# Performance work log

Hardware: AMD Instinct MI355X
Metric: run time of the kernel (lower is better)

Reference implementation:

```python
import jax, jax.numpy as jnp
import numpy as np

N_NODES = 50000
N_EDGES = 1000000
NODE_DIM = 128
EDGE_DIM = 64


def setup_inputs() -> dict:
    key = jax.random.key(0)
    ks = jax.random.split(key, 12)
    s = 1.0 / np.sqrt(EDGE_DIM)
    sn = 1.0 / np.sqrt(NODE_DIM)
    return {
        "x": jax.random.normal(ks[0], (N_NODES, NODE_DIM), jnp.float32),
        "edge_index": jax.random.randint(ks[1], (2, N_EDGES), 0, N_NODES, jnp.int64),
        "edge_attr": jax.random.normal(ks[2], (N_EDGES, EDGE_DIM), jnp.float32),
        # lin_e: edge_dim -> edge_dim
        "We": jax.random.uniform(ks[3], (EDGE_DIM, EDGE_DIM), jnp.float32, -s, s),
        "be": jax.random.uniform(ks[4], (EDGE_DIM,), jnp.float32, -s, s),
        # lin_s: node_dim -> edge_dim
        "Ws": jax.random.uniform(ks[5], (EDGE_DIM, NODE_DIM), jnp.float32, -sn, sn),
        "bs": jax.random.uniform(ks[6], (EDGE_DIM,), jnp.float32, -sn, sn),
        # lin_t: node_dim -> edge_dim
        "Wt": jax.random.uniform(ks[7], (EDGE_DIM, NODE_DIM), jnp.float32, -sn, sn),
        "bt": jax.random.uniform(ks[8], (EDGE_DIM,), jnp.float32, -sn, sn),
        # lin1: edge_dim -> edge_dim
        "W1": jax.random.uniform(ks[9], (EDGE_DIM, EDGE_DIM), jnp.float32, -s, s),
        "b1": jax.random.uniform(ks[10], (EDGE_DIM,), jnp.float32, -s, s),
    }


def reference(x, edge_index, edge_attr, We, be, Ws, bs, Wt, bt, W1, b1):
    # node projections: [N, edge_dim]
    x_s = x @ Ws.T + bs
    x_t = x @ Wt.T + bt
    # fused edge update: lin_e(edge_attr) + gather(x_s, src) + gather(x_t, tgt)
    e = edge_attr @ We.T + be + x_s[edge_index[0]] + x_t[edge_index[1]]  # [E, edge_dim]
    e = jax.nn.gelu(e)
    return e @ W1.T + b1
```

## Files before the change

### kernel.cpp

```cpp
#include <hip/hip_runtime.h>
#include <stdint.h>

#define N_NODES_C 50000
#define N_EDGES_C 1000000
#define NODE_DIM_C 128
#define EDGE_DIM_C 64

typedef __attribute__((ext_vector_type(8))) short short8;
typedef __attribute__((ext_vector_type(4))) float floatx4;

__device__ __forceinline__ short f2bf(float f) {
    union { float f; uint32_t u; } v; v.f = f;
    uint32_t u = v.u;
    uint32_t r = (u + 0x7FFFu + ((u >> 16) & 1u)) >> 16;
    return (short)r;
}

__device__ __forceinline__ float gelu_tanh(float x) {
    float u = x * x;
    float inner = x * (1.0f + 0.044715f * u);
    float z = 1.5957691216057308f * inner;
    float ez = __expf(-z);
    return x / (1.0f + ez);
}

__global__ __launch_bounds__(256) void node_proj_kernel(
    const float* __restrict__ x,
    const float* __restrict__ Ws, const float* __restrict__ bs,
    const float* __restrict__ Wt, const float* __restrict__ bt,
    float* __restrict__ xs, float* __restrict__ xt)
{
    __shared__ __align__(16) short ws_frag[4][4][64][8];
    __shared__ __align__(16) short wt_frag[4][4][64][8];

    const int tid = threadIdx.x;
    for (int eidx = tid; eidx < 1024; eidx += 256) {
        int t = eidx >> 8;
        int s = (eidx >> 6) & 3;
        int l = eidx & 63;
        int n = t * 16 + (l & 15);
        int kb = s * 32 + ((l >> 4) << 3);
        const float* wsr = Ws + n * NODE_DIM_C + kb;
        const float* wtr = Wt + n * NODE_DIM_C + kb;
#pragma unroll
        for (int i = 0; i < 8; ++i) {
            ws_frag[t][s][l][i] = f2bf(wsr[i]);
            wt_frag[t][s][l][i] = f2bf(wtr[i]);
        }
    }
    __syncthreads();

    const int wave = tid >> 6, lane = tid & 63;
    const int m = lane & 15, q = lane >> 4;
    const int base = blockIdx.x * 64 + wave * 16;
    const int arow = base + m;

    floatx4 accS[4], accT[4];
    const floatx4 zero = {0.f, 0.f, 0.f, 0.f};
#pragma unroll
    for (int t = 0; t < 4; ++t) { accS[t] = zero; accT[t] = zero; }

#pragma unroll
    for (int s = 0; s < 4; ++s) {
        short8 a;
        if (arow < N_NODES_C) {
            const float4* ap = (const float4*)(x + arow * NODE_DIM_C + s * 32 + q * 8);
            float4 a0 = ap[0], a1 = ap[1];
            a[0] = f2bf(a0.x); a[1] = f2bf(a0.y); a[2] = f2bf(a0.z); a[3] = f2bf(a0.w);
            a[4] = f2bf(a1.x); a[5] = f2bf(a1.y); a[6] = f2bf(a1.z); a[7] = f2bf(a1.w);
        } else {
#pragma unroll
            for (int i = 0; i < 8; ++i) a[i] = 0;
        }
#pragma unroll
        for (int t = 0; t < 4; ++t) {
            short8 bS = *(const short8*)ws_frag[t][s][lane];
            short8 bT = *(const short8*)wt_frag[t][s][lane];
            accS[t] = __builtin_amdgcn_mfma_f32_16x16x32_bf16(a, bS, accS[t], 0, 0, 0);
            accT[t] = __builtin_amdgcn_mfma_f32_16x16x32_bf16(a, bT, accT[t], 0, 0, 0);
        }
    }

#pragma unroll
    for (int t = 0; t < 4; ++t) {
        int col = t * 16 + m;
        float bsv = bs[col], btv = bt[col];
#pragma unroll
        for (int r = 0; r < 4; ++r) {
            int n = base + q * 4 + r;
            if (n < N_NODES_C) {
                xs[n * EDGE_DIM_C + col] = accS[t][r] + bsv;
                xt[n * EDGE_DIM_C + col] = accT[t][r] + btv;
            }
        }
    }
}

__global__ __launch_bounds__(256) void edge_mlp_kernel(
    const float* __restrict__ ea, const int* __restrict__ ei,
    const float* __restrict__ We, const float* __restrict__ be,
    const float* __restrict__ W1, const float* __restrict__ b1,
    const float* __restrict__ xs, const float* __restrict__ xt,
    float* __restrict__ out)
{
    __shared__ __align__(16) short we_frag[4][2][64][8];
    __shared__ __align__(16) short w1_frag[4][2][64][8];
    __shared__ __align__(16) short pbuf[4][16][72];

    const int tid = threadIdx.x;
    for (int eidx = tid; eidx < 512; eidx += 256) {
        int t = eidx >> 7;
        int s = (eidx >> 6) & 1;
        int l = eidx & 63;
        int n = t * 16 + (l & 15);
        int kb = s * 32 + ((l >> 4) << 3);
        const float* wer = We + n * EDGE_DIM_C + kb;
        const float* w1r = W1 + n * EDGE_DIM_C + kb;
#pragma unroll
        for (int i = 0; i < 8; ++i) {
            we_frag[t][s][l][i] = f2bf(wer[i]);
            w1_frag[t][s][l][i] = f2bf(w1r[i]);
        }
    }
    __syncthreads();

    const int wave = tid >> 6, lane = tid & 63;
    const int m = lane & 15, q = lane >> 4;
    const int* __restrict__ src = ei;
    const int* __restrict__ tgt = ei + N_EDGES_C;

    float bev[4], b1v[4];
#pragma unroll
    for (int t = 0; t < 4; ++t) { bev[t] = be[t * 16 + m]; b1v[t] = b1[t * 16 + m]; }

    const floatx4 zero = {0.f, 0.f, 0.f, 0.f};
    const int nchunks = N_EDGES_C / 64;

    for (int chunk = blockIdx.x; chunk < nchunks; chunk += gridDim.x) {
        const int base = chunk * 64 + wave * 16;

        floatx4 acc[4];
#pragma unroll
        for (int t = 0; t < 4; ++t) acc[t] = zero;
#pragma unroll
        for (int s = 0; s < 2; ++s) {
            const float4* ap = (const float4*)(ea + (base + m) * EDGE_DIM_C + s * 32 + q * 8);
            float4 a0 = ap[0], a1 = ap[1];
            short8 a;
            a[0] = f2bf(a0.x); a[1] = f2bf(a0.y); a[2] = f2bf(a0.z); a[3] = f2bf(a0.w);
            a[4] = f2bf(a1.x); a[5] = f2bf(a1.y); a[6] = f2bf(a1.z); a[7] = f2bf(a1.w);
#pragma unroll
            for (int t = 0; t < 4; ++t) {
                short8 b = *(const short8*)we_frag[t][s][lane];
                acc[t] = __builtin_amdgcn_mfma_f32_16x16x32_bf16(a, b, acc[t], 0, 0, 0);
            }
        }

        int sidx[4], tidx[4];
#pragma unroll
        for (int r = 0; r < 4; ++r) {
            int e = base + q * 4 + r;
            int si = src[e], ti = tgt[e];
            sidx[r] = min(max(si, 0), N_NODES_C - 1);
            tidx[r] = min(max(ti, 0), N_NODES_C - 1);
        }
#pragma unroll
        for (int t = 0; t < 4; ++t) {
            int col = t * 16 + m;
#pragma unroll
            for (int r = 0; r < 4; ++r) {
                float c = acc[t][r] + bev[t]
                        + xs[sidx[r] * EDGE_DIM_C + col]
                        + xt[tidx[r] * EDGE_DIM_C + col];
                pbuf[wave][q * 4 + r][col] = f2bf(gelu_tanh(c));
            }
        }

        floatx4 acc2[4];
#pragma unroll
        for (int t = 0; t < 4; ++t) acc2[t] = zero;
#pragma unroll
        for (int s = 0; s < 2; ++s) {
            short8 a2 = *(const short8*)&pbuf[wave][m][s * 32 + q * 8];
#pragma unroll
            for (int t = 0; t < 4; ++t) {
                short8 b = *(const short8*)w1_frag[t][s][lane];
                acc2[t] = __builtin_amdgcn_mfma_f32_16x16x32_bf16(a2, b, acc2[t], 0, 0, 0);
            }
        }

#pragma unroll
        for (int t = 0; t < 4; ++t) {
            int col = t * 16 + m;
#pragma unroll
            for (int r = 0; r < 4; ++r) {
                int e = base + q * 4 + r;
                out[e * EDGE_DIM_C + col] = acc2[t][r] + b1v[t];
            }
        }
    }
}

extern "C" void kernel_launch(void* const* d_in, const int* in_sizes, int n_in,
                              void* d_out, int out_size, void* d_ws, size_t ws_size,
                              hipStream_t stream) {
    const float* x   = (const float*)d_in[0];
    const int*   ei  = (const int*)d_in[1];
    const float* ea  = (const float*)d_in[2];
    const float* We  = (const float*)d_in[3];
    const float* be  = (const float*)d_in[4];
    const float* Ws  = (const float*)d_in[5];
    const float* bs  = (const float*)d_in[6];
    const float* Wt  = (const float*)d_in[7];
    const float* bt  = (const float*)d_in[8];
    const float* W1  = (const float*)d_in[9];
    const float* b1  = (const float*)d_in[10];
    float* out = (float*)d_out;

    float* xs = (float*)d_ws;
    float* xt = xs + (size_t)N_NODES_C * EDGE_DIM_C;

    dim3 blk(256);
    dim3 grid_nodes((N_NODES_C + 63) / 64);
    node_proj_kernel<<<grid_nodes, blk, 0, stream>>>(x, Ws, bs, Wt, bt, xs, xt);

    dim3 grid_edges(3125);
    edge_mlp_kernel<<<grid_edges, blk, 0, stream>>>(ea, ei, We, be, W1, b1, xs, xt, out);
}
```

Before: 515.0 us.

## Store node projections in bf16, vectorize gathers and output via LDS staging

Node projections xs/xt are now stored as bf16, which halves the gather traffic. Each lane gathers full 16-element row segments with 16-byte loads instead of scalar strided loads. Edge indices for the next chunk are prefetched, the gathered sums are staged through shared memory, and the output tile is transposed through LDS so it can be written with float4 stores. It also adds an occupancy hint in the launch bounds, at the cost of extra LDS use and bf16 rounding of the projections.

```diff
diff --git a/kernel.cpp b/kernel.cpp
--- a/kernel.cpp
+++ b/kernel.cpp
@@ -14,6 +14,12 @@
     uint32_t u = v.u;
     uint32_t r = (u + 0x7FFFu + ((u >> 16) & 1u)) >> 16;
     return (short)r;
+}
+
+__device__ __forceinline__ float bf2f(short s) {
+    union { uint32_t u; float f; } v;
+    v.u = ((uint32_t)(uint16_t)s) << 16;
+    return v.f;
 }
 
 __device__ __forceinline__ float gelu_tanh(float x) {
@@ -28,7 +34,7 @@
     const float* __restrict__ x,
     const float* __restrict__ Ws, const float* __restrict__ bs,
     const float* __restrict__ Wt, const float* __restrict__ bt,
-    float* __restrict__ xs, float* __restrict__ xt)
+    ushort* __restrict__ xs, ushort* __restrict__ xt)
 {
     __shared__ __align__(16) short ws_frag[4][4][64][8];
     __shared__ __align__(16) short wt_frag[4][4][64][8];
@@ -64,7 +70,7 @@
     for (int s = 0; s < 4; ++s) {
         short8 a;
         if (arow < N_NODES_C) {
-            const float4* ap = (const float4*)(x + arow * NODE_DIM_C + s * 32 + q * 8);
+            const float4* ap = (const float4*)(x + (size_t)arow * NODE_DIM_C + s * 32 + q * 8);
             float4 a0 = ap[0], a1 = ap[1];
             a[0] = f2bf(a0.x); a[1] = f2bf(a0.y); a[2] = f2bf(a0.z); a[3] = f2bf(a0.w);
             a[4] = f2bf(a1.x); a[5] = f2bf(a1.y); a[6] = f2bf(a1.z); a[7] = f2bf(a1.w);
@@ -89,23 +95,24 @@
         for (int r = 0; r < 4; ++r) {
             int n = base + q * 4 + r;
             if (n < N_NODES_C) {
-                xs[n * EDGE_DIM_C + col] = accS[t][r] + bsv;
-                xt[n * EDGE_DIM_C + col] = accT[t][r] + btv;
-            }
-        }
-    }
-}
-
-__global__ __launch_bounds__(256) void edge_mlp_kernel(
+                xs[(size_t)n * EDGE_DIM_C + col] = (ushort)f2bf(accS[t][r] + bsv);
+                xt[(size_t)n * EDGE_DIM_C + col] = (ushort)f2bf(accT[t][r] + btv);
+            }
+        }
+    }
+}
+
+__global__ __launch_bounds__(256, 3) void edge_mlp_kernel(
     const float* __restrict__ ea, const int* __restrict__ ei,
     const float* __restrict__ We, const float* __restrict__ be,
     const float* __restrict__ W1, const float* __restrict__ b1,
-    const float* __restrict__ xs, const float* __restrict__ xt,
+    const ushort* __restrict__ xs, const ushort* __restrict__ xt,
     float* __restrict__ out)
 {
     __shared__ __align__(16) short we_frag[4][2][64][8];
     __shared__ __align__(16) short w1_frag[4][2][64][8];
     __shared__ __align__(16) short pbuf[4][16][72];
+    __shared__ __align__(16) float gsum[4][16][68];
 
     const int tid = threadIdx.x;
     for (int eidx = tid; eidx < 512; eidx += 256) {
@@ -126,6 +133,7 @@
 
     const int wave = tid >> 6, lane = tid & 63;
     const int m = lane & 15, q = lane >> 4;
+    const int g_r = lane >> 2, g_c = lane & 3;
     const int* __restrict__ src = ei;
     const int* __restrict__ tgt = ei + N_EDGES_C;
 
@@ -136,15 +144,32 @@
     const floatx4 zero = {0.f, 0.f, 0.f, 0.f};
     const int nchunks = N_EDGES_C / 64;
 
-    for (int chunk = blockIdx.x; chunk < nchunks; chunk += gridDim.x) {
+    int chunk = blockIdx.x;
+    int si = src[chunk * 64 + wave * 16 + g_r];
+    int ti = tgt[chunk * 64 + wave * 16 + g_r];
+
+    for (; chunk < nchunks; chunk += gridDim.x) {
         const int base = chunk * 64 + wave * 16;
 
+        int sic = min(max(si, 0), N_NODES_C - 1);
+        int tic = min(max(ti, 0), N_NODES_C - 1);
+        const short8* xsp = (const short8*)(xs + (size_t)sic * EDGE_DIM_C + g_c * 16);
+        const short8* xtp = (const short8*)(xt + (size_t)tic * EDGE_DIM_C + g_c * 16);
+        short8 gs0 = xsp[0], gs1 = xsp[1];
+        short8 gt0 = xtp[0], gt1 = xtp[1];
+
+        {
+            int en = min((chunk + (int)gridDim.x) * 64 + wave * 16 + g_r, N_EDGES_C - 1);
+            si = src[en];
+            ti = tgt[en];
+        }
+
         floatx4 acc[4];
 #pragma unroll
         for (int t = 0; t < 4; ++t) acc[t] = zero;
 #pragma unroll
         for (int s = 0; s < 2; ++s) {
-            const float4* ap = (const float4*)(ea + (base + m) * EDGE_DIM_C + s * 32 + q * 8);
+            const float4* ap = (const float4*)(ea + (size_t)(base + m) * EDGE_DIM_C + s * 32 + q * 8);
             float4 a0 = ap[0], a1 = ap[1];
             short8 a;
             a[0] = f2bf(a0.x); a[1] = f2bf(a0.y); a[2] = f2bf(a0.z); a[3] = f2bf(a0.w);
@@ -156,23 +181,29 @@
             }
         }
 
-        int sidx[4], tidx[4];
-#pragma unroll
-        for (int r = 0; r < 4; ++r) {
-            int e = base + q * 4 + r;
-            int si = src[e], ti = tgt[e];
-            sidx[r] = min(max(si, 0), N_NODES_C - 1);
-            tidx[r] = min(max(ti, 0), N_NODES_C - 1);
-        }
+        {
+            float* grow = &gsum[wave][g_r][g_c * 16];
+            float4 s0, s1, s2, s3;
+            s0.x = bf2f(gs0[0]) + bf2f(gt0[0]); s0.y = bf2f(gs0[1]) + bf2f(gt0[1]);
+            s0.z = bf2f(gs0[2]) + bf2f(gt0[2]); s0.w = bf2f(gs0[3]) + bf2f(gt0[3]);
+            s1.x = bf2f(gs0[4]) + bf2f(gt0[4]); s1.y = bf2f(gs0[5]) + bf2f(gt0[5]);
+            s1.z = bf2f(gs0[6]) + bf2f(gt0[6]); s1.w = bf2f(gs0[7]) + bf2f(gt0[7]);
+            s2.x = bf2f(gs1[0]) + bf2f(gt1[0]); s2.y = bf2f(gs1[1]) + bf2f(gt1[1]);
+            s2.z = bf2f(gs1[2]) + bf2f(gt1[2]); s2.w = bf2f(gs1[3]) + bf2f(gt1[3]);
+            s3.x = bf2f(gs1[4]) + bf2f(gt1[4]); s3.y = bf2f(gs1[5]) + bf2f(gt1[5]);
+            s3.z = bf2f(gs1[6]) + bf2f(gt1[6]); s3.w = bf2f(gs1[7]) + bf2f(gt1[7]);
+            ((float4*)grow)[0] = s0; ((float4*)grow)[1] = s1;
+            ((float4*)grow)[2] = s2; ((float4*)grow)[3] = s3;
+        }
+
 #pragma unroll
         for (int t = 0; t < 4; ++t) {
             int col = t * 16 + m;
 #pragma unroll
             for (int r = 0; r < 4; ++r) {
-                float c = acc[t][r] + bev[t]
-                        + xs[sidx[r] * EDGE_DIM_C + col]
-                        + xt[tidx[r] * EDGE_DIM_C + col];
-                pbuf[wave][q * 4 + r][col] = f2bf(gelu_tanh(c));
+                int row = q * 4 + r;
+                float c = acc[t][r] + bev[t] + gsum[wave][row][col];
+                pbuf[wave][row][col] = f2bf(gelu_tanh(c));
             }
         }
 
@@ -191,12 +222,16 @@
 
 #pragma unroll
         for (int t = 0; t < 4; ++t) {
-            int col = t * 16 + m;
 #pragma unroll
             for (int r = 0; r < 4; ++r) {
-                int e = base + q * 4 + r;
-                out[e * EDGE_DIM_C + col] = acc2[t][r] + b1v[t];
-            }
+                gsum[wave][q * 4 + r][t * 16 + m] = acc2[t][r] + b1v[t];
+            }
+        }
+        {
+            const float4* orow = (const float4*)&gsum[wave][g_r][g_c * 16];
+            float4 o0 = orow[0], o1 = orow[1], o2 = orow[2], o3 = orow[3];
+            float4* op = (float4*)(out + (size_t)(base + g_r) * EDGE_DIM_C + g_c * 16);
+            op[0] = o0; op[1] = o1; op[2] = o2; op[3] = o3;
         }
     }
 }
@@ -217,8 +252,8 @@
     const float* b1  = (const float*)d_in[10];
     float* out = (float*)d_out;
 
-    float* xs = (float*)d_ws;
-    float* xt = xs + (size_t)N_NODES_C * EDGE_DIM_C;
+    ushort* xs = (ushort*)d_ws;
+    ushort* xt = xs + (size_t)N_NODES_C * EDGE_DIM_C;
 
     dim3 blk(256);
     dim3 grid_nodes((N_NODES_C + 63) / 64);
```

After: 518.5 us. Within noise of the previous version (+0.7%).
